# Kernel optimization log

Hardware: AMD Instinct MI355X
Metric: run time of the kernel (lower is better)

The kernel has to match this reference:

```python
import jax, jax.numpy as jnp
import numpy as np

N_MAP, N_ACT, B, E_PER, D = 131072, 1024, 16, 16384, 128
MAP_PER, ACT_PER = N_MAP // B, N_ACT // B
E = B * E_PER
EPS = 1e-5  # torch GroupNorm default eps


def _gn(x, g, b):
    # GroupNorm(1, C) on [N, C]: per-row normalization over channels
    m = jnp.mean(x, -1, keepdims=True)
    v = jnp.mean((x - m) ** 2, -1, keepdims=True)
    return (x - m) * jax.lax.rsqrt(v + EPS) * g + b


def _lin_gn(x, W, g, b, act=True):
    # LaneGCN Linear: nn.Linear(bias=False) -> GroupNorm(1, n_out) -> optional ReLU
    y = _gn(x @ W.T, g, b)
    return jax.nn.relu(y) if act else y


def setup_inputs() -> dict:
    key = jax.random.key(0)
    keys = iter(jax.random.split(key, 64))
    nrm = lambda shape, s=1.0: jax.random.normal(next(keys), shape, jnp.float32) * s
    uni = lambda shape, s=1.0: jax.random.uniform(next(keys), shape, jnp.float32) * s
    inp = {}
    inp['feat'] = nrm((N_MAP, D))
    inp['turn'] = nrm((N_MAP, 2))
    inp['control'] = uni((N_MAP,))
    inp['intersect'] = uni((N_MAP,))
    inp['map_ctrs'] = uni((N_MAP, 2), 100.0)
    inp['actors'] = nrm((N_ACT, D))
    inp['actor_ctrs'] = uni((N_ACT, 2), 100.0)
    # fixed within-scene edge list (stands in for the distance-threshold nonzero)
    rng = np.random.default_rng(0)
    hi = np.concatenate([rng.integers(b * MAP_PER, (b + 1) * MAP_PER, E_PER) for b in range(B)])
    wi = np.concatenate([rng.integers(b * ACT_PER, (b + 1) * ACT_PER, E_PER) for b in range(B)])
    inp['hi'] = jnp.asarray(hi, jnp.int32)
    inp['wi'] = jnp.asarray(wi, jnp.int32)
    # parameters
    W = lambda *s: nrm(s, 0.02)
    g_ = lambda *s: 1.0 + nrm(s, 0.05)
    b_ = lambda *s: nrm(s, 0.05)
    inp['meta_W'], inp['meta_g'], inp['meta_b'] = W(D, D + 4), g_(D), b_(D)
    inp['dW1'], inp['db1'] = W(2, D, 2), b_(2, D)
    inp['dW2'], inp['dg2'], inp['dbt2'] = W(2, D, D), g_(2, D), b_(2, D)
    inp['qW'], inp['qg'], inp['qb'] = W(2, D, D), g_(2, D), b_(2, D)
    inp['cW1'], inp['cg1'], inp['cb1'] = W(2, D, 3 * D), g_(2, D), b_(2, D)
    inp['cW2'] = W(2, D, D)
    inp['aW'] = W(2, D, D)
    inp['ng_g'], inp['ng_b'] = g_(2, D), b_(2, D)
    inp['lW'], inp['lg'], inp['lb'] = W(2, D, D), g_(2, D), b_(2, D)
    return inp


def reference(feat, turn, control, intersect, map_ctrs, actors, actor_ctrs, hi, wi,
              meta_W, meta_g, meta_b, dW1, db1, dW2, dg2, dbt2, qW, qg, qb,
              cW1, cg1, cb1, cW2, aW, ng_g, ng_b, lW, lg, lb):
    # meta fuse: concat(feat, turn, control, intersect) -> Linear+GN+ReLU
    meta = jnp.concatenate([feat, turn, control[:, None], intersect[:, None]], axis=1)
    feat = _lin_gn(meta, meta_W, meta_g, meta_b)
    for i in range(2):  # two Att blocks
        res = feat
        # dist branch: raw ctr offsets -> Linear(2,n_ctx)+ReLU -> Linear+GN+ReLU
        d = map_ctrs[hi] - actor_ctrs[wi]                       # [E, 2]
        d = jax.nn.relu(d @ dW1[i].T + db1[i])                  # [E, D]
        d = _lin_gn(d, dW2[i], dg2[i], dbt2[i])
        q = _lin_gn(feat[hi], qW[i], qg[i], qb[i])              # query on gathered agts
        c = jnp.concatenate([d, q, actors[wi]], axis=1)         # [E, 3D]
        c = _lin_gn(c, cW1[i], cg1[i], cb1[i])
        c = c @ cW2[i].T                                        # bias-free Linear
        a = feat @ aW[i].T                                      # self path, bias-free
        a = a.at[hi].add(c)                                     # scatter-add messages
        a = jax.nn.relu(_gn(a, ng_g[i], ng_b[i]))
        a = _lin_gn(a, lW[i], lg[i], lb[i], act=False)
        feat = jax.nn.relu(a + res)                             # use_relu=True
    return feat
```

## Files before the change

kernel.cpp:

```cpp
#include <hip/hip_runtime.h>
#include <stdint.h>

typedef unsigned short u16;
typedef __bf16 bf16x8 __attribute__((ext_vector_type(8)));
typedef float f32x4 __attribute__((ext_vector_type(4)));

#define MFMA(a, b, c) __builtin_amdgcn_mfma_f32_16x16x32_bf16(a, b, c, 0, 0, 0)

__device__ __forceinline__ u16 f2bf(float f) {
    union { float f; unsigned u; } v; v.f = f;
    unsigned r = v.u + 0x7fffu + ((v.u >> 16) & 1u);
    return (u16)(r >> 16);
}
__device__ __forceinline__ float bf2f(u16 h) {
    union { unsigned u; float f; } v; v.u = ((unsigned)h) << 16; return v.f;
}
__device__ __forceinline__ bf16x8 as_frag(uint4 u) {
    union { uint4 u; bf16x8 b; } v; v.u = u; return v.b;
}
__device__ __forceinline__ bf16x8 ldg_frag(const u16* p) {
    return as_frag(*reinterpret_cast<const uint4*>(p));
}
__device__ __forceinline__ int rowmap(int t, int i) {
    return 32 * (t >> 1) + 8 * (i >> 2) + 4 * (t & 1) + (i & 3);
}

template <int SRC_LDU>
__device__ __forceinline__ void stage128(const u16* __restrict__ src, u16* dst, int tid, int nt) {
    for (int c = tid; c < 2048; c += nt) {
        int row = c >> 4, j = c & 15;
        int js = (j & 8) | ((j ^ row) & 7);
        *reinterpret_cast<uint4*>(dst + row * 128 + js * 8) =
            *reinterpret_cast<const uint4*>(src + row * SRC_LDU + j * 8);
    }
}
__device__ __forceinline__ bf16x8 lds_w(const u16* base, int row, int byteoff) {
    int off = row * 256 + (byteoff ^ ((row & 7) << 4));
    return as_frag(*reinterpret_cast<const uint4*>(reinterpret_cast<const char*>(base) + off));
}

template <int KT>
__device__ __forceinline__ void gemm_acc(const bf16x8* a, const u16* __restrict__ W, int ldw,
                                         f32x4* acc, int c16, int q4) {
#pragma unroll
    for (int n = 0; n < 8; n++) {
        const u16* wp = W + (size_t)(n * 16 + c16) * ldw + q4 * 8;
#pragma unroll
        for (int k = 0; k < KT; k++) {
            bf16x8 b = ldg_frag(wp + k * 32);
            acc[n] = MFMA(a[k], b, acc[n]);
        }
    }
}

__device__ __forceinline__ void gn_t(f32x4* acc, const float* __restrict__ gb, bool relu, int q4) {
    float s = 0.f, s2 = 0.f;
#pragma unroll
    for (int t = 0; t < 8; t++)
#pragma unroll
        for (int r = 0; r < 4; r++) { float x = acc[t][r]; s += x; s2 = fmaf(x, x, s2); }
    s += __shfl_xor(s, 16, 64); s += __shfl_xor(s, 32, 64);
    s2 += __shfl_xor(s2, 16, 64); s2 += __shfl_xor(s2, 32, 64);
    float mean = s * (1.f / 128.f);
    float var = fmaf(s2, 1.f / 128.f, -mean * mean);
    float rstd = rsqrtf(var + 1e-5f);
#pragma unroll
    for (int t = 0; t < 8; t++) {
        const float4* g4 = reinterpret_cast<const float4*>(gb + (t * 16 + q4 * 4) * 2);
        float4 p01 = g4[0], p23 = g4[1];
        float gv[4] = {p01.x, p01.z, p23.x, p23.z};
        float bv[4] = {p01.y, p01.w, p23.y, p23.w};
#pragma unroll
        for (int r = 0; r < 4; r++) {
            float y = fmaf((acc[t][r] - mean) * rstd, gv[r], bv[r]);
            acc[t][r] = relu ? fmaxf(y, 0.f) : y;
        }
    }
}

__device__ __forceinline__ bf16x8 pack_frag(f32x4 lo, f32x4 hi) {
    union { u16 s[8]; bf16x8 b; } t;
#pragma unroll
    for (int j = 0; j < 4; j++) { t.s[j] = f2bf(lo[j]); t.s[4 + j] = f2bf(hi[j]); }
    return t.b;
}

__device__ __forceinline__ void gn_c(f32x4* acc, const float* __restrict__ g,
                                     const float* __restrict__ b, bool relu, int c16) {
    float gs[8], bs[8];
#pragma unroll
    for (int n = 0; n < 8; n++) { gs[n] = g[n * 16 + c16]; bs[n] = b[n * 16 + c16]; }
#pragma unroll
    for (int r = 0; r < 4; r++) {
        float s = 0.f, s2 = 0.f;
#pragma unroll
        for (int n = 0; n < 8; n++) { float x = acc[n][r]; s += x; s2 = fmaf(x, x, s2); }
#pragma unroll
        for (int m = 1; m < 16; m <<= 1) { s += __shfl_xor(s, m, 64); s2 += __shfl_xor(s2, m, 64); }
        float mean = s * (1.f / 128.f);
        float var = fmaf(s2, 1.f / 128.f, -mean * mean);
        float rstd = rsqrtf(var + 1e-5f);
#pragma unroll
        for (int n = 0; n < 8; n++) {
            float y = fmaf((acc[n][r] - mean) * rstd, gs[n], bs[n]);
            acc[n][r] = relu ? fmaxf(y, 0.f) : y;
        }
    }
}

__global__ __launch_bounds__(256) void k_prep(
    const float* __restrict__ dW2s, const float* __restrict__ qWs, const float* __restrict__ cW1s,
    const float* __restrict__ cW2s, const float* __restrict__ aWs, const float* __restrict__ lWs,
    const float* __restrict__ metaW,
    const float* __restrict__ dW1s, const float* __restrict__ db1s,
    const float* __restrict__ dg2s, const float* __restrict__ dbt2s,
    const float* __restrict__ qgs, const float* __restrict__ qbs,
    const float* __restrict__ cg1s, const float* __restrict__ cb1s,
    u16* __restrict__ o_dW2p, u16* __restrict__ o_qWp, u16* __restrict__ o_cW10,
    u16* __restrict__ o_cW1q, u16* __restrict__ o_cW1a,
    u16* __restrict__ o_cW2, u16* __restrict__ o_aW, u16* __restrict__ o_lW,
    u16* __restrict__ o_mWf, float* __restrict__ o_mWe,
    float* __restrict__ o_dw1p, float* __restrict__ o_gb) {
    int idx = blockIdx.x * 256 + threadIdx.x;
    if (idx >= 281600) return;
    if (idx < 32768) {
        int i = idx >> 14, rem = idx & 16383, ro = rem >> 7, col = rem & 127;
        o_dW2p[idx] = f2bf(dW2s[i * 16384 + rowmap(ro >> 4, ro & 15) * 128 + col]);
    } else if (idx < 65536) {
        int j = idx - 32768, i = j >> 14, rem = j & 16383, ro = rem >> 7, col = rem & 127;
        o_qWp[j] = f2bf(qWs[i * 16384 + rowmap(ro >> 4, ro & 15) * 128 + col]);
    } else if (idx < 98304) {
        int j = idx - 65536, i = j >> 14, rem = j & 16383, ro = rem >> 7, col = rem & 127;
        o_cW10[j] = f2bf(cW1s[i * 49152 + rowmap(ro >> 4, ro & 15) * 384 + col]);
    } else if (idx < 131072) {
        int j = idx - 98304, i = j >> 14, rem = j & 16383, ro = rem >> 7, col = rem & 127;
        o_cW1q[j] = f2bf(cW1s[i * 49152 + rowmap(ro >> 4, ro & 15) * 384 + 128 + col]);
    } else if (idx < 163840) {
        int j = idx - 131072, i = j >> 14, rem = j & 16383, ro = rem >> 7, col = rem & 127;
        o_cW1a[j] = f2bf(cW1s[i * 49152 + rowmap(ro >> 4, ro & 15) * 384 + 256 + col]);
    } else if (idx < 196608) { int j = idx - 163840; o_cW2[j] = f2bf(cW2s[j]); }
    else if (idx < 229376) { int j = idx - 196608; o_aW[j] = f2bf(aWs[j]); }
    else if (idx < 262144) { int j = idx - 229376; o_lW[j] = f2bf(lWs[j]); }
    else if (idx < 278528) { int j = idx - 262144; o_mWf[j] = f2bf(metaW[(j >> 7) * 132 + (j & 127)]); }
    else if (idx < 279040) { int j = idx - 278528; o_mWe[j] = metaW[(j >> 2) * 132 + 128 + (j & 3)]; }
    else if (idx < 280064) {
        int j = idx - 279040, i = j >> 9, col = (j >> 2) & 127, t = j & 3;
        float v = (t == 0) ? dW1s[i * 256 + col * 2]
                : (t == 1) ? dW1s[i * 256 + col * 2 + 1]
                : (t == 2) ? db1s[i * 128 + col] : 0.f;
        o_dw1p[j] = v;
    } else {
        int j = idx - 280064;
        int tb = j >> 9, rem = j & 511, i = rem >> 8, q = rem & 255, o = q >> 1, f = q & 1;
        const float* gsrc = (tb == 0) ? dg2s : (tb == 1) ? qgs : cg1s;
        const float* bsrc = (tb == 0) ? dbt2s : (tb == 1) ? qbs : cb1s;
        int src = i * 128 + rowmap(o >> 4, o & 15);
        o_gb[j] = f ? bsrc[src] : gsrc[src];
    }
}

__global__ __launch_bounds__(256) void k_meta(
    const float* __restrict__ feat, const float* __restrict__ turn,
    const float* __restrict__ ctrl, const float* __restrict__ inter,
    const u16* __restrict__ mWf, const float* __restrict__ mWe,
    const float* __restrict__ g, const float* __restrict__ b, u16* __restrict__ out) {
    int lane = threadIdx.x & 63, wv = threadIdx.x >> 6;
    int c16 = lane & 15, q4 = lane >> 4;
    int m0 = (blockIdx.x * 4 + wv) * 16;
    bf16x8 a[4];
    const float* xr = feat + (size_t)(m0 + c16) * 128 + q4 * 8;
#pragma unroll
    for (int k = 0; k < 4; k++) {
        float4 u0 = *reinterpret_cast<const float4*>(xr + k * 32);
        float4 u1 = *reinterpret_cast<const float4*>(xr + k * 32 + 4);
        union { u16 s[8]; bf16x8 b; } t;
        t.s[0] = f2bf(u0.x); t.s[1] = f2bf(u0.y); t.s[2] = f2bf(u0.z); t.s[3] = f2bf(u0.w);
        t.s[4] = f2bf(u1.x); t.s[5] = f2bf(u1.y); t.s[6] = f2bf(u1.z); t.s[7] = f2bf(u1.w);
        a[k] = t.b;
    }
    f32x4 acc[8] = {};
    gemm_acc<4>(a, mWf, 128, acc, c16, q4);
#pragma unroll
    for (int r = 0; r < 4; r++) {
        int row = m0 + q4 * 4 + r;
        float t0 = turn[2 * row], t1 = turn[2 * row + 1];
        float cv = ctrl[row], iv = inter[row];
#pragma unroll
        for (int n = 0; n < 8; n++) {
            int col = n * 16 + c16;
            float4 we = reinterpret_cast<const float4*>(mWe)[col];
            acc[n][r] += t0 * we.x + t1 * we.y + cv * we.z + iv * we.w;
        }
    }
    gn_c(acc, g, b, true, c16);
#pragma unroll
    for (int r = 0; r < 4; r++) {
        size_t row = m0 + q4 * 4 + r;
#pragma unroll
        for (int n = 0; n < 8; n++) out[row * 128 + n * 16 + c16] = f2bf(acc[n][r]);
    }
}

__global__ __launch_bounds__(256) void k_act(
    const float* __restrict__ actors, const u16* __restrict__ cW1ap, u16* __restrict__ ac_out) {
    int lane = threadIdx.x & 63, wv = threadIdx.x >> 6;
    int c16 = lane & 15, q4 = lane >> 4;
    int b = (int)blockIdx.x;
    int i = b >> 4;
    int row = ((b & 15) * 4 + wv) * 16 + c16;
    const float* xr = actors + (size_t)row * 128 + q4 * 8;
    bf16x8 f[4];
#pragma unroll
    for (int k = 0; k < 4; k++) {
        union { u16 s[8]; uint4 u; } t;
#pragma unroll
        for (int j = 0; j < 8; j++) t.s[j] = f2bf(xr[k * 32 + j]);
        f[k] = as_frag(t.u);
    }
    const u16* Wp = cW1ap + i * 16384;
    f32x4 acc[8] = {};
#pragma unroll
    for (int k = 0; k < 4; k++)
#pragma unroll
        for (int t = 0; t < 8; t++) {
            bf16x8 a = ldg_frag(Wp + (size_t)(t * 16 + c16) * 128 + k * 32 + q4 * 8);
            acc[t] = MFMA(a, f[k], acc[t]);
        }
    u16* dst = ac_out + (size_t)i * 131072 + (size_t)row * 128 + q4 * 8;
#pragma unroll
    for (int T = 0; T < 4; T++) {
        bf16x8 p = pack_frag(acc[2 * T], acc[2 * T + 1]);
        union { bf16x8 b; uint4 u; } v; v.b = p;
        *reinterpret_cast<uint4*>(dst + T * 32) = v.u;
    }
}

__global__ __launch_bounds__(256) void k_nodeA(
    const u16* __restrict__ featb, const u16* __restrict__ qWp, const u16* __restrict__ aW,
    const float* __restrict__ gb_q, const u16* __restrict__ cW1qp,
    u16* __restrict__ qc_out, u16* __restrict__ a_out) {
    int lane = threadIdx.x & 63, wv = threadIdx.x >> 6;
    int c16 = lane & 15, q4 = lane >> 4;
    int m0 = (blockIdx.x * 4 + wv) * 16;
    bf16x8 f[4];
    const u16* xr = featb + (size_t)(m0 + c16) * 128 + q4 * 8;
#pragma unroll
    for (int k = 0; k < 4; k++) f[k] = ldg_frag(xr + k * 32);
    f32x4 acca[8] = {};
    gemm_acc<4>(f, aW, 128, acca, c16, q4);
#pragma unroll
    for (int r = 0; r < 4; r++) {
        size_t row = m0 + q4 * 4 + r;
#pragma unroll
        for (int n = 0; n < 8; n++) a_out[row * 128 + n * 16 + c16] = f2bf(acca[n][r]);
    }
    f32x4 accq[8] = {};
#pragma unroll
    for (int k = 0; k < 4; k++)
#pragma unroll
        for (int t = 0; t < 8; t++) {
            bf16x8 a = ldg_frag(qWp + (size_t)(t * 16 + c16) * 128 + k * 32 + q4 * 8);
            accq[t] = MFMA(a, f[k], accq[t]);
        }
    gn_t(accq, gb_q, true, q4);
    bf16x8 qf[4];
#pragma unroll
    for (int k = 0; k < 4; k++) qf[k] = pack_frag(accq[2 * k], accq[2 * k + 1]);
    f32x4 acc2[8] = {};
#pragma unroll
    for (int k = 0; k < 4; k++)
#pragma unroll
        for (int t = 0; t < 8; t++) {
            bf16x8 a = ldg_frag(cW1qp + (size_t)(t * 16 + c16) * 128 + k * 32 + q4 * 8);
            acc2[t] = MFMA(a, qf[k], acc2[t]);
        }
    u16* dst = qc_out + (size_t)(m0 + c16) * 128 + q4 * 8;
#pragma unroll
    for (int T = 0; T < 4; T++) {
        bf16x8 p = pack_frag(acc2[2 * T], acc2[2 * T + 1]);
        union { bf16x8 b; uint4 u; } v; v.b = p;
        *reinterpret_cast<uint4*>(dst + T * 32) = v.u;
    }
}

__global__ __launch_bounds__(256) void k_edge(
    const int* __restrict__ hi, const int* __restrict__ wi,
    const float* __restrict__ mctr, const float* __restrict__ actr,
    const float* __restrict__ dw1p, const u16* __restrict__ dW2p,
    const float* __restrict__ gb_d2,
    const u16* __restrict__ qc, const u16* __restrict__ ac,
    const u16* __restrict__ cW10p, const float* __restrict__ gb_c1,
    const u16* __restrict__ cW2, u16* __restrict__ a_out) {
    __shared__ u16 s0[16384];
    int tid = threadIdx.x;
    int lane = tid & 63, wv = tid >> 6;
    int c16 = lane & 15, q4 = lane >> 4;
    int bid = (int)blockIdx.x;
    bid = (bid & 7) * 256 + (bid >> 3);
    int ebase = bid * 128 + wv * 32;
    int h0 = hi[ebase + c16], w0 = wi[ebase + c16];
    int h1 = hi[ebase + 16 + c16], w1 = wi[ebase + 16 + c16];
    stage128<128>(dW2p, s0, tid, 256);
    union F8 { bf16x8 b; uint4 u; u16 s[8]; };
    F8 qg0[4], qg1[4], ag0[4], ag1[4];
#pragma unroll
    for (int T = 0; T < 4; T++) {
        qg0[T].b = ldg_frag(qc + (size_t)h0 * 128 + T * 32 + q4 * 8);
        qg1[T].b = ldg_frag(qc + (size_t)h1 * 128 + T * 32 + q4 * 8);
        ag0[T].b = ldg_frag(ac + (size_t)w0 * 128 + T * 32 + q4 * 8);
        ag1[T].b = ldg_frag(ac + (size_t)w1 * 128 + T * 32 + q4 * 8);
    }
    float dx0 = mctr[2 * h0] - actr[2 * w0], dy0 = mctr[2 * h0 + 1] - actr[2 * w0 + 1];
    float dx1 = mctr[2 * h1] - actr[2 * w1], dy1 = mctr[2 * h1 + 1] - actr[2 * w1 + 1];
    bf16x8 bd0[4], bd1[4];
    const float4* w4p = reinterpret_cast<const float4*>(dw1p);
#pragma unroll
    for (int k = 0; k < 4; k++) {
        union { u16 s[8]; uint4 u; } t0, t1;
#pragma unroll
        for (int j = 0; j < 8; j++) {
            float4 w4 = w4p[k * 32 + q4 * 8 + j];
            t0.s[j] = f2bf(fmaxf(fmaf(dx0, w4.x, fmaf(dy0, w4.y, w4.z)), 0.f));
            t1.s[j] = f2bf(fmaxf(fmaf(dx1, w4.x, fmaf(dy1, w4.y, w4.z)), 0.f));
        }
        bd0[k] = as_frag(t0.u); bd1[k] = as_frag(t1.u);
    }
    __syncthreads();
    f32x4 accA[8] = {}, accB[8] = {};
#pragma unroll
    for (int k = 0; k < 4; k++)
#pragma unroll
        for (int t = 0; t < 8; t++) {
            bf16x8 a = lds_w(s0, t * 16 + c16, k * 64 + q4 * 16);
            accA[t] = MFMA(a, bd0[k], accA[t]);
            accB[t] = MFMA(a, bd1[k], accB[t]);
        }
    gn_t(accA, gb_d2, true, q4);
    gn_t(accB, gb_d2, true, q4);
    bf16x8 d2f0[4], d2f1[4];
#pragma unroll
    for (int k = 0; k < 4; k++) {
        d2f0[k] = pack_frag(accA[2 * k], accA[2 * k + 1]);
        d2f1[k] = pack_frag(accB[2 * k], accB[2 * k + 1]);
    }
    __syncthreads();
    stage128<128>(cW10p, s0, tid, 256);
    __syncthreads();
    f32x4 cA[8] = {}, cB[8] = {};
#pragma unroll
    for (int k = 0; k < 4; k++)
#pragma unroll
        for (int t = 0; t < 8; t++) {
            bf16x8 a = lds_w(s0, t * 16 + c16, k * 64 + q4 * 16);
            cA[t] = MFMA(a, d2f0[k], cA[t]);
            cB[t] = MFMA(a, d2f1[k], cB[t]);
        }
#pragma unroll
    for (int t = 0; t < 8; t++) {
        int T = t >> 1, base = 4 * (t & 1);
#pragma unroll
        for (int r = 0; r < 4; r++) {
            cA[t][r] += bf2f(qg0[T].s[base + r]) + bf2f(ag0[T].s[base + r]);
            cB[t][r] += bf2f(qg1[T].s[base + r]) + bf2f(ag1[T].s[base + r]);
        }
    }
    gn_t(cA, gb_c1, true, q4);
    gn_t(cB, gb_c1, true, q4);
    bf16x8 ba0[4], ba1[4];
#pragma unroll
    for (int k = 0; k < 4; k++) {
        ba0[k] = pack_frag(cA[2 * k], cA[2 * k + 1]);
        ba1[k] = pack_frag(cB[2 * k], cB[2 * k + 1]);
    }
    __syncthreads();
    stage128<128>(cW2, s0, tid, 256);
    __syncthreads();
    f32x4 oA[8] = {}, oB[8] = {};
#pragma unroll
    for (int k = 0; k < 4; k++)
#pragma unroll
        for (int n = 0; n < 8; n++) {
            bf16x8 b = lds_w(s0, n * 16 + c16, k * 64 + q4 * 16);
            oA[n] = MFMA(ba0[k], b, oA[n]);
            oB[n] = MFMA(ba1[k], b, oB[n]);
        }
#pragma unroll
    for (int r = 0; r < 4; r++) {
        int hr0 = hi[ebase + q4 * 4 + r];
        int hr1 = hi[ebase + 16 + q4 * 4 + r];
        u16* d0 = a_out + (size_t)hr0 * 128 + (c16 & ~1);
        u16* d1 = a_out + (size_t)hr1 * 128 + (c16 & ~1);
#pragma unroll
        for (int n = 0; n < 8; n++) {
            float pA = __shfl_xor(oA[n][r], 1, 64);
            float pB = __shfl_xor(oB[n][r], 1, 64);
            bool even = !(c16 & 1);
            float loA = even ? oA[n][r] : pA, hiA = even ? pA : oA[n][r];
            float loB = even ? oB[n][r] : pB, hiB = even ? pB : oB[n][r];
            unsigned pkA = (unsigned)f2bf(loA) | ((unsigned)f2bf(hiA) << 16);
            unsigned pkB = (unsigned)f2bf(loB) | ((unsigned)f2bf(hiB) << 16);
            if ((n & 1) == (c16 & 1)) {
                asm volatile("global_atomic_pk_add_bf16 %0, %1, off"
                             :: "v"(d0 + n * 16), "v"(pkA) : "memory");
                asm volatile("global_atomic_pk_add_bf16 %0, %1, off"
                             :: "v"(d1 + n * 16), "v"(pkB) : "memory");
            }
        }
    }
}

__global__ __launch_bounds__(256) void k_nodeB(
    const u16* a_in, const float* __restrict__ gg, const float* __restrict__ gb,
    const u16* __restrict__ lW, const float* __restrict__ lg, const float* __restrict__ lb,
    const u16* __restrict__ res, u16* out_bf, float* __restrict__ out_f32) {
    int lane = threadIdx.x & 63, wv = threadIdx.x >> 6;
    int c16 = lane & 15, q4 = lane >> 4;
    int m0 = (blockIdx.x * 4 + wv) * 16;
    const u16* xr = a_in + (size_t)(m0 + c16) * 128 + q4 * 8;
    float x[32];
#pragma unroll
    for (int k = 0; k < 4; k++) {
        union { uint4 u; u16 s[8]; } v;
        v.u = *reinterpret_cast<const uint4*>(xr + k * 32);
#pragma unroll
        for (int j = 0; j < 8; j++) x[k * 8 + j] = bf2f(v.s[j]);
    }
    float s = 0.f, s2 = 0.f;
#pragma unroll
    for (int t = 0; t < 32; t++) { s += x[t]; s2 = fmaf(x[t], x[t], s2); }
    s += __shfl_xor(s, 16, 64); s += __shfl_xor(s, 32, 64);
    s2 += __shfl_xor(s2, 16, 64); s2 += __shfl_xor(s2, 32, 64);
    float mean = s * (1.f / 128.f);
    float var = fmaf(s2, 1.f / 128.f, -mean * mean);
    float rstd = rsqrtf(var + 1e-5f);
    bf16x8 a[4];
#pragma unroll
    for (int k = 0; k < 4; k++) {
        float4 g0 = *reinterpret_cast<const float4*>(gg + k * 32 + q4 * 8);
        float4 g1 = *reinterpret_cast<const float4*>(gg + k * 32 + q4 * 8 + 4);
        float4 b0 = *reinterpret_cast<const float4*>(gb + k * 32 + q4 * 8);
        float4 b1 = *reinterpret_cast<const float4*>(gb + k * 32 + q4 * 8 + 4);
        float gv[8] = {g0.x, g0.y, g0.z, g0.w, g1.x, g1.y, g1.z, g1.w};
        float bv[8] = {b0.x, b0.y, b0.z, b0.w, b1.x, b1.y, b1.z, b1.w};
        union { u16 s[8]; bf16x8 b; } t;
#pragma unroll
        for (int j = 0; j < 8; j++) {
            float y = fmaf((x[k * 8 + j] - mean) * rstd, gv[j], bv[j]);
            t.s[j] = f2bf(fmaxf(y, 0.f));
        }
        a[k] = t.b;
    }
    f32x4 acc[8] = {};
    gemm_acc<4>(a, lW, 128, acc, c16, q4);
    gn_c(acc, lg, lb, false, c16);
#pragma unroll
    for (int r = 0; r < 4; r++) {
        size_t row = m0 + q4 * 4 + r;
#pragma unroll
        for (int n = 0; n < 8; n++) {
            int col = n * 16 + c16;
            float y = acc[n][r] + bf2f(res[row * 128 + col]);
            y = fmaxf(y, 0.f);
            if (out_bf) out_bf[row * 128 + col] = f2bf(y);
            else out_f32[row * 128 + col] = y;
        }
    }
}

extern "C" void kernel_launch(void* const* d_in, const int* in_sizes, int n_in,
                              void* d_out, int out_size, void* d_ws, size_t ws_size,
                              hipStream_t stream) {
    const float* feat = (const float*)d_in[0];
    const float* turn = (const float*)d_in[1];
    const float* ctrl = (const float*)d_in[2];
    const float* inter = (const float*)d_in[3];
    const float* mctr = (const float*)d_in[4];
    const float* actors = (const float*)d_in[5];
    const float* actr = (const float*)d_in[6];
    const int* hi = (const int*)d_in[7];
    const int* wi = (const int*)d_in[8];
    const float* metaW = (const float*)d_in[9];
    const float* metag = (const float*)d_in[10];
    const float* metab = (const float*)d_in[11];
    const float* dW1 = (const float*)d_in[12];
    const float* db1 = (const float*)d_in[13];
    const float* dW2 = (const float*)d_in[14];
    const float* dg2 = (const float*)d_in[15];
    const float* dbt2 = (const float*)d_in[16];
    const float* qW = (const float*)d_in[17];
    const float* qg = (const float*)d_in[18];
    const float* qb = (const float*)d_in[19];
    const float* cW1 = (const float*)d_in[20];
    const float* cg1 = (const float*)d_in[21];
    const float* cb1 = (const float*)d_in[22];
    const float* cW2 = (const float*)d_in[23];
    const float* aW = (const float*)d_in[24];
    const float* ngg = (const float*)d_in[25];
    const float* ngb = (const float*)d_in[26];
    const float* lW = (const float*)d_in[27];
    const float* lg = (const float*)d_in[28];
    const float* lb = (const float*)d_in[29];

    char* ws = (char*)d_ws;
    u16* feat0 = (u16*)(ws);
    u16* feat1 = (u16*)(ws + 33554432);
    u16* qcbuf = (u16*)(ws + 67108864);
    u16* acbuf = (u16*)(ws + 100663296);
    u16* wdW2p = (u16*)(ws + 101187584);
    u16* wqWp = (u16*)(ws + 101253120);
    u16* wcW10 = (u16*)(ws + 101318656);
    u16* wcW1q = (u16*)(ws + 101384192);
    u16* wcW1a = (u16*)(ws + 101449728);
    u16* wcW2 = (u16*)(ws + 101515264);
    u16* waW = (u16*)(ws + 101580800);
    u16* wlW = (u16*)(ws + 101646336);
    u16* wmWf = (u16*)(ws + 101711872);
    float* wmWe = (float*)(ws + 101744640);
    float* wdw1p = (float*)(ws + 101746688);
    float* gball = (float*)(ws + 101750784);

    k_prep<<<1100, 256, 0, stream>>>(dW2, qW, cW1, cW2, aW, lW, metaW, dW1, db1,
                                     dg2, dbt2, qg, qb, cg1, cb1,
                                     wdW2p, wqWp, wcW10, wcW1q, wcW1a, wcW2, waW, wlW,
                                     wmWf, wmWe, wdw1p, gball);
    k_meta<<<2048, 256, 0, stream>>>(feat, turn, ctrl, inter, wmWf, wmWe, metag, metab, feat0);
    k_act<<<32, 256, 0, stream>>>(actors, wcW1a, acbuf);
    for (int i = 0; i < 2; i++) {
        const u16* fcur = i ? feat1 : feat0;
        u16* abuf = i ? feat0 : feat1;
        k_nodeA<<<2048, 256, 0, stream>>>(fcur, wqWp + i * 16384, waW + i * 16384,
                                          gball + 512 + i * 256, wcW1q + i * 16384,
                                          qcbuf, abuf);
        k_edge<<<2048, 256, 0, stream>>>(hi, wi, mctr, actr, wdw1p + i * 512, wdW2p + i * 16384,
                                         gball + i * 256, qcbuf, acbuf + i * 131072,
                                         wcW10 + i * 16384, gball + 1024 + i * 256,
                                         wcW2 + i * 16384, abuf);
        k_nodeB<<<2048, 256, 0, stream>>>(abuf, ngg + i * 128, ngb + i * 128, wlW + i * 16384,
                                          lg + i * 128, lb + i * 128, fcur,
                                          i ? nullptr : feat1, i ? (float*)d_out : nullptr);
    }
}
```

Measured before the change: 704.7 us.

## Halve edges per wave in k_edge and read cW2 from global

Each wave now handles 16 edges instead of 32, and the grid doubles to 4096 blocks with launch bounds asking for 4 blocks per SM. This cuts accumulator register pressure so more waves can be resident. The third GEMM now reads cW2 fragments straight from global/L2 instead of staging them in LDS, which removes one staging pass and two barriers. In exchange, dW2 and cW10 are staged twice as often across the grid and each LDS weight fragment is reused for half as many MFMAs.

```diff
diff --git a/kernel.cpp b/kernel.cpp
--- a/kernel.cpp
+++ b/kernel.cpp
@@ -283,7 +283,7 @@
     }
 }
 
-__global__ __launch_bounds__(256) void k_edge(
+__global__ __launch_bounds__(256, 4) void k_edge(
     const int* __restrict__ hi, const int* __restrict__ wi,
     const float* __restrict__ mctr, const float* __restrict__ actr,
     const float* __restrict__ dw1p, const u16* __restrict__ dW2p,
@@ -296,114 +296,88 @@
     int lane = tid & 63, wv = tid >> 6;
     int c16 = lane & 15, q4 = lane >> 4;
     int bid = (int)blockIdx.x;
-    bid = (bid & 7) * 256 + (bid >> 3);
-    int ebase = bid * 128 + wv * 32;
+    bid = (bid & 7) * 512 + (bid >> 3);
+    int ebase = bid * 64 + wv * 16;
     int h0 = hi[ebase + c16], w0 = wi[ebase + c16];
-    int h1 = hi[ebase + 16 + c16], w1 = wi[ebase + 16 + c16];
     stage128<128>(dW2p, s0, tid, 256);
     union F8 { bf16x8 b; uint4 u; u16 s[8]; };
-    F8 qg0[4], qg1[4], ag0[4], ag1[4];
+    F8 qg[4], ag[4];
 #pragma unroll
     for (int T = 0; T < 4; T++) {
-        qg0[T].b = ldg_frag(qc + (size_t)h0 * 128 + T * 32 + q4 * 8);
-        qg1[T].b = ldg_frag(qc + (size_t)h1 * 128 + T * 32 + q4 * 8);
-        ag0[T].b = ldg_frag(ac + (size_t)w0 * 128 + T * 32 + q4 * 8);
-        ag1[T].b = ldg_frag(ac + (size_t)w1 * 128 + T * 32 + q4 * 8);
+        qg[T].b = ldg_frag(qc + (size_t)h0 * 128 + T * 32 + q4 * 8);
+        ag[T].b = ldg_frag(ac + (size_t)w0 * 128 + T * 32 + q4 * 8);
     }
     float dx0 = mctr[2 * h0] - actr[2 * w0], dy0 = mctr[2 * h0 + 1] - actr[2 * w0 + 1];
-    float dx1 = mctr[2 * h1] - actr[2 * w1], dy1 = mctr[2 * h1 + 1] - actr[2 * w1 + 1];
-    bf16x8 bd0[4], bd1[4];
+    bf16x8 bd0[4];
     const float4* w4p = reinterpret_cast<const float4*>(dw1p);
 #pragma unroll
     for (int k = 0; k < 4; k++) {
-        union { u16 s[8]; uint4 u; } t0, t1;
+        union { u16 s[8]; uint4 u; } t0;
 #pragma unroll
         for (int j = 0; j < 8; j++) {
             float4 w4 = w4p[k * 32 + q4 * 8 + j];
             t0.s[j] = f2bf(fmaxf(fmaf(dx0, w4.x, fmaf(dy0, w4.y, w4.z)), 0.f));
-            t1.s[j] = f2bf(fmaxf(fmaf(dx1, w4.x, fmaf(dy1, w4.y, w4.z)), 0.f));
-        }
-        bd0[k] = as_frag(t0.u); bd1[k] = as_frag(t1.u);
+        }
+        bd0[k] = as_frag(t0.u);
     }
     __syncthreads();
-    f32x4 accA[8] = {}, accB[8] = {};
+    f32x4 acc[8] = {};
 #pragma unroll
     for (int k = 0; k < 4; k++)
 #pragma unroll
         for (int t = 0; t < 8; t++) {
             bf16x8 a = lds_w(s0, t * 16 + c16, k * 64 + q4 * 16);
-            accA[t] = MFMA(a, bd0[k], accA[t]);
-            accB[t] = MFMA(a, bd1[k], accB[t]);
-        }
-    gn_t(accA, gb_d2, true, q4);
-    gn_t(accB, gb_d2, true, q4);
-    bf16x8 d2f0[4], d2f1[4];
-#pragma unroll
-    for (int k = 0; k < 4; k++) {
-        d2f0[k] = pack_frag(accA[2 * k], accA[2 * k + 1]);
-        d2f1[k] = pack_frag(accB[2 * k], accB[2 * k + 1]);
-    }
+            acc[t] = MFMA(a, bd0[k], acc[t]);
+        }
+    gn_t(acc, gb_d2, true, q4);
+    bf16x8 d2f[4];
+#pragma unroll
+    for (int k = 0; k < 4; k++) d2f[k] = pack_frag(acc[2 * k], acc[2 * k + 1]);
     __syncthreads();
     stage128<128>(cW10p, s0, tid, 256);
     __syncthreads();
-    f32x4 cA[8] = {}, cB[8] = {};
+#pragma unroll
+    for (int t = 0; t < 8; t++) acc[t] = f32x4{0, 0, 0, 0};
 #pragma unroll
     for (int k = 0; k < 4; k++)
 #pragma unroll
         for (int t = 0; t < 8; t++) {
             bf16x8 a = lds_w(s0, t * 16 + c16, k * 64 + q4 * 16);
-            cA[t] = MFMA(a, d2f0[k], cA[t]);
-            cB[t] = MFMA(a, d2f1[k], cB[t]);
+            acc[t] = MFMA(a, d2f[k], acc[t]);
         }
 #pragma unroll
     for (int t = 0; t < 8; t++) {
         int T = t >> 1, base = 4 * (t & 1);
 #pragma unroll
-        for (int r = 0; r < 4; r++) {
-            cA[t][r] += bf2f(qg0[T].s[base + r]) + bf2f(ag0[T].s[base + r]);
-            cB[t][r] += bf2f(qg1[T].s[base + r]) + bf2f(ag1[T].s[base + r]);
-        }
-    }
-    gn_t(cA, gb_c1, true, q4);
-    gn_t(cB, gb_c1, true, q4);
-    bf16x8 ba0[4], ba1[4];
-#pragma unroll
-    for (int k = 0; k < 4; k++) {
-        ba0[k] = pack_frag(cA[2 * k], cA[2 * k + 1]);
-        ba1[k] = pack_frag(cB[2 * k], cB[2 * k + 1]);
-    }
-    __syncthreads();
-    stage128<128>(cW2, s0, tid, 256);
-    __syncthreads();
-    f32x4 oA[8] = {}, oB[8] = {};
+        for (int r = 0; r < 4; r++)
+            acc[t][r] += bf2f(qg[T].s[base + r]) + bf2f(ag[T].s[base + r]);
+    }
+    gn_t(acc, gb_c1, true, q4);
+    bf16x8 ba[4];
+#pragma unroll
+    for (int k = 0; k < 4; k++) ba[k] = pack_frag(acc[2 * k], acc[2 * k + 1]);
+#pragma unroll
+    for (int t = 0; t < 8; t++) acc[t] = f32x4{0, 0, 0, 0};
 #pragma unroll
     for (int k = 0; k < 4; k++)
 #pragma unroll
         for (int n = 0; n < 8; n++) {
-            bf16x8 b = lds_w(s0, n * 16 + c16, k * 64 + q4 * 16);
-            oA[n] = MFMA(ba0[k], b, oA[n]);
-            oB[n] = MFMA(ba1[k], b, oB[n]);
+            bf16x8 b = ldg_frag(cW2 + (size_t)(n * 16 + c16) * 128 + k * 32 + q4 * 8);
+            acc[n] = MFMA(ba[k], b, acc[n]);
         }
 #pragma unroll
     for (int r = 0; r < 4; r++) {
         int hr0 = hi[ebase + q4 * 4 + r];
-        int hr1 = hi[ebase + 16 + q4 * 4 + r];
         u16* d0 = a_out + (size_t)hr0 * 128 + (c16 & ~1);
-        u16* d1 = a_out + (size_t)hr1 * 128 + (c16 & ~1);
 #pragma unroll
         for (int n = 0; n < 8; n++) {
-            float pA = __shfl_xor(oA[n][r], 1, 64);
-            float pB = __shfl_xor(oB[n][r], 1, 64);
+            float pA = __shfl_xor(acc[n][r], 1, 64);
             bool even = !(c16 & 1);
-            float loA = even ? oA[n][r] : pA, hiA = even ? pA : oA[n][r];
-            float loB = even ? oB[n][r] : pB, hiB = even ? pB : oB[n][r];
+            float loA = even ? acc[n][r] : pA, hiA = even ? pA : acc[n][r];
             unsigned pkA = (unsigned)f2bf(loA) | ((unsigned)f2bf(hiA) << 16);
-            unsigned pkB = (unsigned)f2bf(loB) | ((unsigned)f2bf(hiB) << 16);
             if ((n & 1) == (c16 & 1)) {
                 asm volatile("global_atomic_pk_add_bf16 %0, %1, off"
                              :: "v"(d0 + n * 16), "v"(pkA) : "memory");
-                asm volatile("global_atomic_pk_add_bf16 %0, %1, off"
-                             :: "v"(d1 + n * 16), "v"(pkB) : "memory");
             }
         }
     }
@@ -531,7 +505,7 @@
         k_nodeA<<<2048, 256, 0, stream>>>(fcur, wqWp + i * 16384, waW + i * 16384,
                                           gball + 512 + i * 256, wcW1q + i * 16384,
                                           qcbuf, abuf);
-        k_edge<<<2048, 256, 0, stream>>>(hi, wi, mctr, actr, wdw1p + i * 512, wdW2p + i * 16384,
+        k_edge<<<4096, 256, 0, stream>>>(hi, wi, mctr, actr, wdw1p + i * 512, wdW2p + i * 16384,
                                          gball + i * 256, qcbuf, acbuf + i * 131072,
                                          wcW10 + i * 16384, gball + 1024 + i * 256,
                                          wcW2 + i * 16384, abuf);
```

New measurement: 755.9 us. 7.3% more time.
